# Kernel optimization log

Hardware: AMD Instinct MI355X
Metric: run time of the kernel (lower is better)

## Reference

```python
import jax, jax.numpy as jnp
import numpy as np

B, T, I, H, L, O = 8192, 204, 5, 24, 10, 612

def setup_inputs() -> dict:
    key = jax.random.key(0)
    ks = jax.random.split(key, 10)
    s_ih = 1.0 / np.sqrt(H)
    inp = {
        "x": jax.random.normal(ks[0], (B, T, I), dtype=jnp.float32),
        # torch nn.LSTM params: weight_ih_l0 [4H,I], weight_hh_l0 [4H,H], biases [4H]
        "W_ih": jax.random.uniform(ks[1], (4 * H, I), jnp.float32, -s_ih, s_ih),
        "W_hh": jax.random.uniform(ks[2], (4 * H, H), jnp.float32, -s_ih, s_ih),
        "b_ih": jax.random.uniform(ks[3], (4 * H,), jnp.float32, -s_ih, s_ih),
        "b_hh": jax.random.uniform(ks[4], (4 * H,), jnp.float32, -s_ih, s_ih),
        "fc0_w": jax.random.uniform(ks[5], (L, H * T), jnp.float32, -1 / np.sqrt(H * T), 1 / np.sqrt(H * T)),
        "fc0_b": jax.random.uniform(ks[6], (L,), jnp.float32, -1 / np.sqrt(H * T), 1 / np.sqrt(H * T)),
        "out_w": jax.random.uniform(ks[7], (O, L), jnp.float32, -1 / np.sqrt(L), 1 / np.sqrt(L)),
        "out_b": jax.random.uniform(ks[8], (O,), jnp.float32, -1 / np.sqrt(L), 1 / np.sqrt(L)),
    }
    return inp

def _lstm_forward(x, W_ih, W_hh, b_ih, b_hh):
    # Precompute input projections for all timesteps: [B,T,4H] -> time-major [T,B,4H]
    x_proj = jnp.einsum("bti,gi->btg", x, W_ih) + b_ih
    x_proj = jnp.swapaxes(x_proj, 0, 1)
    h0 = jnp.zeros((x.shape[0], W_hh.shape[1]), x.dtype)
    c0 = jnp.zeros_like(h0)

    def step(carry, xt):
        h, c = carry
        gates = xt + h @ W_hh.T + b_hh  # [B,4H]; torch gate order i,f,g,o
        i, f, g, o = jnp.split(gates, 4, axis=-1)
        c = jax.nn.sigmoid(f) * c + jax.nn.sigmoid(i) * jnp.tanh(g)
        h = jax.nn.sigmoid(o) * jnp.tanh(c)
        return (h, c), h

    _, hs = jax.lax.scan(step, (h0, c0), x_proj)  # hs: [T,B,H]
    return jnp.swapaxes(hs, 0, 1)  # [B,T,H]

def reference(x, W_ih, W_hh, b_ih, b_hh, fc0_w, fc0_b, out_w, out_b):
    h = _lstm_forward(x, W_ih, W_hh, b_ih, b_hh)       # [B,T,H]
    h = h.reshape(h.shape[0], -1)                       # [B, T*H]
    h = jax.nn.relu(h @ fc0_w.T + fc0_b)                # [B, L]
    return h @ out_w.T + out_b                          # [B, O]
```

## Files before the change

### kernel.cpp

```cpp
#include <hip/hip_runtime.h>
#include <math.h>

#define T_  204
#define I_  5
#define H_  24
#define L_  10
#define O_  612
#define Bsz 8192

typedef _Float16 half8 __attribute__((ext_vector_type(8)));
typedef _Float16 half2t __attribute__((ext_vector_type(2)));
typedef float    float4t __attribute__((ext_vector_type(4)));

union U16B { float4t f4; half8 h8; float f[4]; _Float16 h[8]; half2t h2[4]; };

__device__ __forceinline__ float fast_rcp(float x){ return __builtin_amdgcn_rcpf(x); }
__device__ __forceinline__ float fast_ex2(float x){ return __builtin_amdgcn_exp2f(x); }
__device__ __forceinline__ half2t pk2(float a, float b){
    return __builtin_bit_cast(half2t, __builtin_amdgcn_cvt_pkrtz(a, b));
}

#define MFMA16(a,b,c) __builtin_amdgcn_mfma_f32_16x16x32_f16((a),(b),(c),0,0,0)

#define L2E  1.44269504f
#define L2E2 2.88539008f

__device__ __forceinline__ float sigm2(float x){ return fast_rcp(1.f + fast_ex2(x * -L2E)); }
__device__ __forceinline__ float tanh2(float x){ return 2.f * fast_rcp(1.f + fast_ex2(x * -L2E2)) - 1.f; }

#define STEP_BARRIER() asm volatile("s_waitcnt lgkmcnt(0)\n\ts_barrier" ::: "memory")

__global__ __launch_bounds__(128)
void lstm_mfma(const float* __restrict__ x,
               const float* __restrict__ W_ih,
               const float* __restrict__ W_hh,
               const float* __restrict__ b_ih,
               const float* __restrict__ b_hh,
               const float* __restrict__ fc0_w,
               const float* __restrict__ fc0_b,
               const float* __restrict__ out_w,
               const float* __restrict__ out_b,
               float* __restrict__ out)
{
    __shared__ __align__(16) _Float16 hL[2*16*40];
    __shared__ __align__(16) _Float16 actL[16*24];

    const int tid  = threadIdx.x;
    const int w    = tid >> 6;
    const int lane = tid & 63;
    const int m = lane & 15;
    const int q = lane >> 4;
    const int elem = blockIdx.x * 16 + m;

    const float4t zf4 = {0.f, 0.f, 0.f, 0.f};

    half8 Ag[3];
    const int g0 = m & 3, ub = 6 * (m >> 2);
    #pragma unroll
    for (int T3 = 0; T3 < 3; ++T3) {
        const int gT = 3*w + T3;
        const int srow = g0 * H_ + ub + gT;
        float wv[8];
        if (q < 3) {
            const float4t* pw = (const float4t*)(W_hh + srow*H_ + 8*q);
            float4t wa = pw[0], wb = pw[1];
            #pragma unroll
            for (int i = 0; i < 4; ++i) { wv[i] = wa[i]; wv[4+i] = wb[i]; }
        } else {
            #pragma unroll
            for (int i = 0; i < 8; ++i) wv[i] = 0.f;
            #pragma unroll
            for (int i = 0; i < I_; ++i) wv[i] = W_ih[srow*I_ + i];
            wv[5] = b_ih[srow] + b_hh[srow];
        }
        U16B tw;
        #pragma unroll
        for (int i = 0; i < 8; ++i) tw.h[i] = (_Float16)wv[i];
        Ag[T3] = tw.h8;
    }

    const int hwIdx = m*40 + 6*q + 3*w;
    const int hrIdx = m*40 + 8*q;

    const float* xp = x + (size_t)elem * (T_*I_);

    const bool fval = (m < 5) && (q < 3);
    const float* fbase = fc0_w + (size_t)(5*w + (m < 5 ? m : 0)) * (T_*H_) + 8*q;
    float4t fA0 = zf4, fA1 = zf4;
    if (fval) {
        fA0 = *(const float4t*)(fbase + 0);
        fA1 = *(const float4t*)(fbase + 4);
    }

    float xA0=0,xA1=0,xA2=0,xA3=0,xA4=0;
    U16B B;
    if (q == 3) {
        B.h2[0] = pk2(xp[0], xp[1]);
        B.h2[1] = pk2(xp[2], xp[3]);
        B.h2[2] = pk2(xp[4], 1.0f);
        B.h2[3] = pk2(0.f, 0.f);
        xA0 = xp[I_+0]; xA1 = xp[I_+1]; xA2 = xp[I_+2]; xA3 = xp[I_+3]; xA4 = xp[I_+4];
    } else {
        B.f4 = zf4;
    }

    float c_[3] = {0.f, 0.f, 0.f};
    float4t accF = zf4;

    #pragma unroll 2
    for (int t = 0; t < T_; ++t) {
        float xB0=0,xB1=0,xB2=0,xB3=0,xB4=0;
        if (q == 3) {
            const int tp2 = (t + 2 < T_) ? t + 2 : T_ - 1;
            const float* xq = xp + tp2*I_;
            xB0 = xq[0]; xB1 = xq[1]; xB2 = xq[2]; xB3 = xq[3]; xB4 = xq[4];
        }
        float4t fB0 = zf4, fB1 = zf4;
        {
            const int tp1 = (t + 1 < T_) ? t + 1 : T_ - 1;
            if (fval) {
                fB0 = *(const float4t*)(fbase + tp1*H_ + 0);
                fB1 = *(const float4t*)(fbase + tp1*H_ + 4);
            }
        }

        float4t D0 = MFMA16(Ag[0], B.h8, zf4);
        float4t D1 = MFMA16(Ag[1], B.h8, zf4);
        float4t D2 = MFMA16(Ag[2], B.h8, zf4);

        const int bofs = (t & 1) * 640;
        {
            float4t D[3] = {D0, D1, D2};
            #pragma unroll
            for (int T3 = 0; T3 < 3; ++T3) {
                const float si = sigm2(D[T3][0]);
                const float sf = sigm2(D[T3][1]);
                const float tg = tanh2(D[T3][2]);
                const float so = sigm2(D[T3][3]);
                c_[T3] = fmaf(sf, c_[T3], si * tg);
                const float hh = so * tanh2(c_[T3]);
                hL[bofs + hwIdx + T3] = (_Float16)hh;
            }
        }

        STEP_BARRIER();

        if (q < 3) {
            B.f4 = *(const float4t*)(&hL[bofs + hrIdx]);
        } else {
            B.h2[0] = pk2(xA0, xA1);
            B.h2[1] = pk2(xA2, xA3);
            B.h2[2] = pk2(xA4, 1.0f);
            B.h2[3] = pk2(0.f, 0.f);
        }

        U16B fF;
        fF.h2[0] = pk2(fA0[0], fA0[1]);
        fF.h2[1] = pk2(fA0[2], fA0[3]);
        fF.h2[2] = pk2(fA1[0], fA1[1]);
        fF.h2[3] = pk2(fA1[2], fA1[3]);
        accF = MFMA16(fF.h8, B.h8, accF);

        fA0 = fB0; fA1 = fB1;
        xA0 = xB0; xA1 = xB1; xA2 = xB2; xA3 = xB3; xA4 = xB4;
    }

    #pragma unroll
    for (int r = 0; r < 4; ++r) {
        const int rid = 4*q + r;
        if (rid < 5) {
            const int l = 5*w + rid;
            const float v = accF[r] + fc0_b[l];
            actL[m*24 + l] = (_Float16)fmaxf(v, 0.f);
        } else if (w == 0 && rid >= 10) {
            actL[m*24 + rid] = (_Float16)0.f;
        }
    }
    __syncthreads();

    U16B Ba;
    if (q < 2) Ba.f4 = *(const float4t*)(&actL[m*24 + 8*q]);
    else       Ba.f4 = zf4;

    for (int Tt = w; Tt < 39; Tt += 2) {
        const int row = 16*Tt + m;
        float w0=0.f,w1=0.f,w2=0.f,w3=0.f,w4=0.f,w5=0.f,w6=0.f,w7=0.f;
        if (row < O_ && q < 2) {
            const float2* p2 = (const float2*)(out_w + row*L_);
            if (q == 0) {
                float2 a = p2[0], b = p2[1], cc = p2[2], dd = p2[3];
                w0=a.x; w1=a.y; w2=b.x; w3=b.y; w4=cc.x; w5=cc.y; w6=dd.x; w7=dd.y;
            } else {
                float2 a = p2[4];
                w0=a.x; w1=a.y;
            }
        }
        U16B Aw;
        Aw.h2[0] = pk2(w0,w1); Aw.h2[1] = pk2(w2,w3);
        Aw.h2[2] = pk2(w4,w5); Aw.h2[3] = pk2(w6,w7);

        float4t dd = MFMA16(Aw.h8, Ba.h8, zf4);

        const int ob = 16*Tt + 4*q;
        if (ob < O_) {
            const float4t bias = *(const float4t*)(out_b + ob);
            #pragma unroll
            for (int r = 0; r < 4; ++r) dd[r] += bias[r];
            *(float4t*)(out + (size_t)elem*O_ + ob) = dd;
        }
    }
}

extern "C" void kernel_launch(void* const* d_in, const int* in_sizes, int n_in,
                              void* d_out, int out_size, void* d_ws, size_t ws_size,
                              hipStream_t stream)
{
    const float* x     = (const float*)d_in[0];
    const float* W_ih  = (const float*)d_in[1];
    const float* W_hh  = (const float*)d_in[2];
    const float* b_ih  = (const float*)d_in[3];
    const float* b_hh  = (const float*)d_in[4];
    const float* fc0_w = (const float*)d_in[5];
    const float* fc0_b = (const float*)d_in[6];
    const float* out_w = (const float*)d_in[7];
    const float* out_b = (const float*)d_in[8];
    float* out = (float*)d_out;
    (void)d_ws; (void)ws_size;

    lstm_mfma<<<dim3(Bsz/16), dim3(128), 0, stream>>>(
        x, W_ih, W_hh, b_ih, b_hh, fc0_w, fc0_b, out_w, out_b, out);
}
```

Measured before the change: 224.9 us.

## Use single-wave blocks handling two batch tiles to drop cross-wave barriers

```diff
diff --git a/kernel.cpp b/kernel.cpp
--- a/kernel.cpp
+++ b/kernel.cpp
@@ -28,9 +28,8 @@
 __device__ __forceinline__ float sigm2(float x){ return fast_rcp(1.f + fast_ex2(x * -L2E)); }
 __device__ __forceinline__ float tanh2(float x){ return 2.f * fast_rcp(1.f + fast_ex2(x * -L2E2)) - 1.f; }
 
-#define STEP_BARRIER() asm volatile("s_waitcnt lgkmcnt(0)\n\ts_barrier" ::: "memory")
-
-__global__ __launch_bounds__(128)
+__global__ __launch_bounds__(64)
+__attribute__((amdgpu_waves_per_eu(1, 2)))
 void lstm_mfma(const float* __restrict__ x,
                const float* __restrict__ W_ih,
                const float* __restrict__ W_hh,
@@ -42,24 +41,22 @@
                const float* __restrict__ out_b,
                float* __restrict__ out)
 {
-    __shared__ __align__(16) _Float16 hL[2*16*40];
-    __shared__ __align__(16) _Float16 actL[16*24];
-
-    const int tid  = threadIdx.x;
-    const int w    = tid >> 6;
-    const int lane = tid & 63;
+    __shared__ __align__(16) _Float16 hL[2][16*40];
+    __shared__ __align__(16) _Float16 actL[2][16*24];
+
+    const int lane = threadIdx.x;
     const int m = lane & 15;
     const int q = lane >> 4;
-    const int elem = blockIdx.x * 16 + m;
+    const int elemA = blockIdx.x * 32 + m;
+    const int elemB = elemA + 16;
 
     const float4t zf4 = {0.f, 0.f, 0.f, 0.f};
 
-    half8 Ag[3];
+    half8 Ag[6];
     const int g0 = m & 3, ub = 6 * (m >> 2);
     #pragma unroll
-    for (int T3 = 0; T3 < 3; ++T3) {
-        const int gT = 3*w + T3;
-        const int srow = g0 * H_ + ub + gT;
+    for (int T6 = 0; T6 < 6; ++T6) {
+        const int srow = g0 * H_ + ub + T6;
         float wv[8];
         if (q < 3) {
             const float4t* pw = (const float4t*)(W_hh + srow*H_ + 8*q);
@@ -76,82 +73,103 @@
         U16B tw;
         #pragma unroll
         for (int i = 0; i < 8; ++i) tw.h[i] = (_Float16)wv[i];
-        Ag[T3] = tw.h8;
-    }
-
-    const int hwIdx = m*40 + 6*q + 3*w;
+        Ag[T6] = tw.h8;
+    }
+
+    const int hwIdx = m*40 + 6*q;
     const int hrIdx = m*40 + 8*q;
 
-    const float* xp = x + (size_t)elem * (T_*I_);
-
-    const bool fval = (m < 5) && (q < 3);
-    const float* fbase = fc0_w + (size_t)(5*w + (m < 5 ? m : 0)) * (T_*H_) + 8*q;
+    const float* xpA = x + (size_t)elemA * (T_*I_);
+    const float* xpB = x + (size_t)elemB * (T_*I_);
+
+    const bool fval = (m < L_) && (q < 3);
+    const float* fbase = fc0_w + (size_t)(m < L_ ? m : 0) * (T_*H_) + 8*q;
     float4t fA0 = zf4, fA1 = zf4;
     if (fval) {
         fA0 = *(const float4t*)(fbase + 0);
         fA1 = *(const float4t*)(fbase + 4);
     }
 
-    float xA0=0,xA1=0,xA2=0,xA3=0,xA4=0;
-    U16B B;
+    U16B BA, BB;
     if (q == 3) {
-        B.h2[0] = pk2(xp[0], xp[1]);
-        B.h2[1] = pk2(xp[2], xp[3]);
-        B.h2[2] = pk2(xp[4], 1.0f);
-        B.h2[3] = pk2(0.f, 0.f);
-        xA0 = xp[I_+0]; xA1 = xp[I_+1]; xA2 = xp[I_+2]; xA3 = xp[I_+3]; xA4 = xp[I_+4];
+        BA.h2[0] = pk2(xpA[0], xpA[1]);
+        BA.h2[1] = pk2(xpA[2], xpA[3]);
+        BA.h2[2] = pk2(xpA[4], 1.0f);
+        BA.h2[3] = pk2(0.f, 0.f);
+        BB.h2[0] = pk2(xpB[0], xpB[1]);
+        BB.h2[1] = pk2(xpB[2], xpB[3]);
+        BB.h2[2] = pk2(xpB[4], 1.0f);
+        BB.h2[3] = pk2(0.f, 0.f);
     } else {
-        B.f4 = zf4;
-    }
-
-    float c_[3] = {0.f, 0.f, 0.f};
-    float4t accF = zf4;
-
-    #pragma unroll 2
+        BA.f4 = zf4; BB.f4 = zf4;
+    }
+
+    float cA[6] = {0,0,0,0,0,0}, cB[6] = {0,0,0,0,0,0};
+    float4t accA = zf4, accB = zf4;
+
     for (int t = 0; t < T_; ++t) {
-        float xB0=0,xB1=0,xB2=0,xB3=0,xB4=0;
+        const int tn = (t + 1 < T_) ? t + 1 : t;
+        float xa[I_] = {0,0,0,0,0}, xb[I_] = {0,0,0,0,0};
         if (q == 3) {
-            const int tp2 = (t + 2 < T_) ? t + 2 : T_ - 1;
-            const float* xq = xp + tp2*I_;
-            xB0 = xq[0]; xB1 = xq[1]; xB2 = xq[2]; xB3 = xq[3]; xB4 = xq[4];
-        }
-        float4t fB0 = zf4, fB1 = zf4;
+            const float* xqa = xpA + tn*I_;
+            const float* xqb = xpB + tn*I_;
+            #pragma unroll
+            for (int i = 0; i < I_; ++i) { xa[i] = xqa[i]; xb[i] = xqb[i]; }
+        }
+        float4t fN0 = zf4, fN1 = zf4;
+        if (fval) {
+            fN0 = *(const float4t*)(fbase + tn*H_ + 0);
+            fN1 = *(const float4t*)(fbase + tn*H_ + 4);
+        }
+
+        float4t DA0 = MFMA16(Ag[0], BA.h8, zf4);
+        float4t DB0 = MFMA16(Ag[0], BB.h8, zf4);
+        float4t DA1 = MFMA16(Ag[1], BA.h8, zf4);
+        float4t DB1 = MFMA16(Ag[1], BB.h8, zf4);
+        float4t DA2 = MFMA16(Ag[2], BA.h8, zf4);
+        float4t DB2 = MFMA16(Ag[2], BB.h8, zf4);
+        float4t DA3 = MFMA16(Ag[3], BA.h8, zf4);
+        float4t DB3 = MFMA16(Ag[3], BB.h8, zf4);
+        float4t DA4 = MFMA16(Ag[4], BA.h8, zf4);
+        float4t DB4 = MFMA16(Ag[4], BB.h8, zf4);
+        float4t DA5 = MFMA16(Ag[5], BA.h8, zf4);
+        float4t DB5 = MFMA16(Ag[5], BB.h8, zf4);
+
         {
-            const int tp1 = (t + 1 < T_) ? t + 1 : T_ - 1;
-            if (fval) {
-                fB0 = *(const float4t*)(fbase + tp1*H_ + 0);
-                fB1 = *(const float4t*)(fbase + tp1*H_ + 4);
+            float4t DA[6] = {DA0, DA1, DA2, DA3, DA4, DA5};
+            float4t DB[6] = {DB0, DB1, DB2, DB3, DB4, DB5};
+            #pragma unroll
+            for (int T6 = 0; T6 < 6; ++T6) {
+                const float siA = sigm2(DA[T6][0]);
+                const float siB = sigm2(DB[T6][0]);
+                const float sfA = sigm2(DA[T6][1]);
+                const float sfB = sigm2(DB[T6][1]);
+                const float tgA = tanh2(DA[T6][2]);
+                const float tgB = tanh2(DB[T6][2]);
+                const float soA = sigm2(DA[T6][3]);
+                const float soB = sigm2(DB[T6][3]);
+                cA[T6] = fmaf(sfA, cA[T6], siA * tgA);
+                cB[T6] = fmaf(sfB, cB[T6], siB * tgB);
+                const float hA = soA * tanh2(cA[T6]);
+                const float hB = soB * tanh2(cB[T6]);
+                hL[0][hwIdx + T6] = (_Float16)hA;
+                hL[1][hwIdx + T6] = (_Float16)hB;
             }
         }
-
-        float4t D0 = MFMA16(Ag[0], B.h8, zf4);
-        float4t D1 = MFMA16(Ag[1], B.h8, zf4);
-        float4t D2 = MFMA16(Ag[2], B.h8, zf4);
-
-        const int bofs = (t & 1) * 640;
-        {
-            float4t D[3] = {D0, D1, D2};
-            #pragma unroll
-            for (int T3 = 0; T3 < 3; ++T3) {
-                const float si = sigm2(D[T3][0]);
-                const float sf = sigm2(D[T3][1]);
-                const float tg = tanh2(D[T3][2]);
-                const float so = sigm2(D[T3][3]);
-                c_[T3] = fmaf(sf, c_[T3], si * tg);
-                const float hh = so * tanh2(c_[T3]);
-                hL[bofs + hwIdx + T3] = (_Float16)hh;
-            }
-        }
-
-        STEP_BARRIER();
+        __builtin_amdgcn_wave_barrier();
 
         if (q < 3) {
-            B.f4 = *(const float4t*)(&hL[bofs + hrIdx]);
+            BA.f4 = *(const float4t*)(&hL[0][hrIdx]);
+            BB.f4 = *(const float4t*)(&hL[1][hrIdx]);
         } else {
-            B.h2[0] = pk2(xA0, xA1);
-            B.h2[1] = pk2(xA2, xA3);
-            B.h2[2] = pk2(xA4, 1.0f);
-            B.h2[3] = pk2(0.f, 0.f);
+            BA.h2[0] = pk2(xa[0], xa[1]);
+            BA.h2[1] = pk2(xa[2], xa[3]);
+            BA.h2[2] = pk2(xa[4], 1.0f);
+            BA.h2[3] = pk2(0.f, 0.f);
+            BB.h2[0] = pk2(xb[0], xb[1]);
+            BB.h2[1] = pk2(xb[2], xb[3]);
+            BB.h2[2] = pk2(xb[4], 1.0f);
+            BB.h2[3] = pk2(0.f, 0.f);
         }
 
         U16B fF;
@@ -159,30 +177,35 @@
         fF.h2[1] = pk2(fA0[2], fA0[3]);
         fF.h2[2] = pk2(fA1[0], fA1[1]);
         fF.h2[3] = pk2(fA1[2], fA1[3]);
-        accF = MFMA16(fF.h8, B.h8, accF);
-
-        fA0 = fB0; fA1 = fB1;
-        xA0 = xB0; xA1 = xB1; xA2 = xB2; xA3 = xB3; xA4 = xB4;
+        accA = MFMA16(fF.h8, BA.h8, accA);
+        accB = MFMA16(fF.h8, BB.h8, accB);
+
+        fA0 = fN0; fA1 = fN1;
     }
 
     #pragma unroll
     for (int r = 0; r < 4; ++r) {
-        const int rid = 4*q + r;
-        if (rid < 5) {
-            const int l = 5*w + rid;
-            const float v = accF[r] + fc0_b[l];
-            actL[m*24 + l] = (_Float16)fmaxf(v, 0.f);
-        } else if (w == 0 && rid >= 10) {
-            actL[m*24 + rid] = (_Float16)0.f;
-        }
-    }
-    __syncthreads();
-
-    U16B Ba;
-    if (q < 2) Ba.f4 = *(const float4t*)(&actL[m*24 + 8*q]);
-    else       Ba.f4 = zf4;
-
-    for (int Tt = w; Tt < 39; Tt += 2) {
+        const int l = 4*q + r;
+        if (l < L_) {
+            const float fb = fc0_b[l];
+            actL[0][m*24 + l] = (_Float16)fmaxf(accA[r] + fb, 0.f);
+            actL[1][m*24 + l] = (_Float16)fmaxf(accB[r] + fb, 0.f);
+        } else if (l < 16) {
+            actL[0][m*24 + l] = (_Float16)0.f;
+            actL[1][m*24 + l] = (_Float16)0.f;
+        }
+    }
+    __builtin_amdgcn_wave_barrier();
+
+    U16B BaA, BaB;
+    if (q < 2) {
+        BaA.f4 = *(const float4t*)(&actL[0][m*24 + 8*q]);
+        BaB.f4 = *(const float4t*)(&actL[1][m*24 + 8*q]);
+    } else {
+        BaA.f4 = zf4; BaB.f4 = zf4;
+    }
+
+    for (int Tt = 0; Tt < 39; ++Tt) {
         const int row = 16*Tt + m;
         float w0=0.f,w1=0.f,w2=0.f,w3=0.f,w4=0.f,w5=0.f,w6=0.f,w7=0.f;
         if (row < O_ && q < 2) {
@@ -199,14 +222,16 @@
         Aw.h2[0] = pk2(w0,w1); Aw.h2[1] = pk2(w2,w3);
         Aw.h2[2] = pk2(w4,w5); Aw.h2[3] = pk2(w6,w7);
 
-        float4t dd = MFMA16(Aw.h8, Ba.h8, zf4);
+        float4t ddA = MFMA16(Aw.h8, BaA.h8, zf4);
+        float4t ddB = MFMA16(Aw.h8, BaB.h8, zf4);
 
         const int ob = 16*Tt + 4*q;
         if (ob < O_) {
             const float4t bias = *(const float4t*)(out_b + ob);
             #pragma unroll
-            for (int r = 0; r < 4; ++r) dd[r] += bias[r];
-            *(float4t*)(out + (size_t)elem*O_ + ob) = dd;
+            for (int r = 0; r < 4; ++r) { ddA[r] += bias[r]; ddB[r] += bias[r]; }
+            *(float4t*)(out + (size_t)elemA*O_ + ob) = ddA;
+            *(float4t*)(out + (size_t)elemB*O_ + ob) = ddB;
         }
     }
 }
@@ -227,6 +252,6 @@
     float* out = (float*)d_out;
     (void)d_ws; (void)ws_size;
 
-    lstm_mfma<<<dim3(Bsz/16), dim3(128), 0, stream>>>(
+    lstm_mfma<<<dim3(Bsz/32), dim3(64), 0, stream>>>(
         x, W_ih, W_hh, b_ih, b_hh, fc0_w, fc0_b, out_w, out_b, out);
 }
```

Result: slower. 327.2 us (+45.5%).
